# Kernel optimization log

Hardware: AMD Instinct MI355X
Metric: run time of the kernel (lower is better)

Reference implementation:

```python
import jax, jax.numpy as jnp
import numpy as np


def bilinear_sampler(img, coords):
    """RAFT-style bilinear sampler: grid_sample(align_corners=True, zero padding)
    at absolute pixel coords. img: (N,C,H,W); coords: (N,Ho,Wo,2) with (x,y).
    Returns (N,C,Ho,Wo)."""
    N, C, H, W = img.shape
    x = coords[..., 0]
    y = coords[..., 1]
    x0f = jnp.floor(x)
    y0f = jnp.floor(y)
    wx = x - x0f  # fractional weights
    wy = y - y0f
    x0 = x0f.astype(jnp.int32)
    y0 = y0f.astype(jnp.int32)
    x1 = x0 + 1
    y1 = y0 + 1
    n = jnp.arange(N)[:, None, None]  # (N,1,1) batch index

    def gather(yi, xi):
        valid = (xi >= 0) & (xi < W) & (yi >= 0) & (yi < H)
        v = img[n, :, jnp.clip(yi, 0, H - 1), jnp.clip(xi, 0, W - 1)]  # (N,Ho,Wo,C)
        return v * valid[..., None].astype(img.dtype)

    out = (gather(y0, x0) * ((1 - wy) * (1 - wx))[..., None]
           + gather(y0, x1) * ((1 - wy) * wx)[..., None]
           + gather(y1, x0) * (wy * (1 - wx))[..., None]
           + gather(y1, x1) * (wy * wx)[..., None])
    return out.transpose(0, 3, 1, 2)


def setup_inputs() -> dict:
    key = jax.random.key(0)
    k1, k2, k3 = jax.random.split(key, 3)
    B, H, W, heads = 4, 64, 64, 1
    cost_maps = jax.random.normal(k1, (B * H * W, heads, H, W), dtype=jnp.float32)
    # pixel coords uniform in [0, W-1]
    coords0 = jax.random.uniform(k2, (B, 2, H, W), dtype=jnp.float32) * (W - 1)
    coords1 = jax.random.uniform(k3, (B, 2, H, W), dtype=jnp.float32) * (W - 1)
    return {"cost_maps": cost_maps, "coords0": coords0, "coords1": coords1}


def reference(cost_maps, coords0, coords1):
    BH1W1, heads, H2, W2 = cost_maps.shape
    B, _, H1, W1 = coords1.shape
    # first gather: sample each (h1,w1,head) cost map at coords1
    cm = cost_maps.reshape(B, H1 * W1 * heads, H2, W2)
    corr = bilinear_sampler(cm, coords1.transpose(0, 2, 3, 1))  # (B, H1*W1*heads, H1, W1)
    # rearrange 'b (h1 w1 heads) h2 w2 -> (b h2 w2) heads h1 w1'
    corr = corr.reshape(B, H1, W1, heads, H2, W2)
    corr = corr.transpose(0, 4, 5, 3, 1, 2).reshape(B * H2 * W2, heads, H1, W1)
    # second gather: 9x9 window around coords0 (faithful to torch meshgrid(dy,dx))
    r = 4
    dx = jnp.linspace(-r, r, 2 * r + 1, dtype=jnp.float32)
    dy = jnp.linspace(-r, r, 2 * r + 1, dtype=jnp.float32)
    delta = jnp.stack(jnp.meshgrid(dy, dx, indexing="ij"), axis=-1)  # (9,9,2)
    centroid = coords0.transpose(0, 2, 3, 1).reshape(BH1W1, 1, 1, 2)
    coords = centroid + delta[None]  # (BH1W1, 9, 9, 2)
    corr = bilinear_sampler(corr, coords)  # (BH1W1, heads, 9, 9)
    out = corr.reshape(B, H1, W1, -1).transpose(0, 3, 1, 2)  # (B, heads*81, H1, W1)
    return out
```

## Files before the change

kernel.cpp:

```cpp
#include <hip/hip_runtime.h>


#define PIX     16
#define THREADS 256

__global__ __launch_bounds__(THREADS, 4)
void rce_kernel(const float* __restrict__ cost,
                const float* __restrict__ coords0,
                const float* __restrict__ coords1,
                float* __restrict__ out) {
    const int tid = threadIdx.x;
    const int P   = blockIdx.x * PIX;
    const int b   = P >> 12;
    const int i   = (P >> 6) & 63;
    const int j0  = P & 63;

    __shared__ int   s_pos[PIX][4];
    __shared__ float s_w[PIX][4];
    __shared__ int   s_x0i[PIX], s_y0i[PIX];
    __shared__ int   s_rx[PIX][9], s_ry[PIX][9];
    __shared__ float s_fx[PIX][9], s_fy[PIX][9];
    __shared__ float s_F[PIX][101];

    if (tid < PIX) {
        const int j = j0 + tid;
        const int cbase = (b * 2) * 4096 + i * 64 + j;

        float x1 = coords1[cbase];
        float y1 = coords1[cbase + 4096];
        float x1f = floorf(x1), y1f = floorf(y1);
        int   xi = (int)x1f,    yi = (int)y1f;
        float wx = x1 - x1f,    wy = y1 - y1f;
        int x0c = min(max(xi, 0), 63),     x1c = min(max(xi + 1, 0), 63);
        int y0c = min(max(yi, 0), 63),     y1c = min(max(yi + 1, 0), 63);
        float vx0 = ((unsigned)xi       < 64u) ? 1.f : 0.f;
        float vx1 = ((unsigned)(xi + 1) < 64u) ? 1.f : 0.f;
        float vy0 = ((unsigned)yi       < 64u) ? 1.f : 0.f;
        float vy1 = ((unsigned)(yi + 1) < 64u) ? 1.f : 0.f;
        s_pos[tid][0] = y0c * 64 + x0c;  s_w[tid][0] = (1.f - wy) * (1.f - wx) * vy0 * vx0;
        s_pos[tid][1] = y0c * 64 + x1c;  s_w[tid][1] = (1.f - wy) * wx         * vy0 * vx1;
        s_pos[tid][2] = y1c * 64 + x0c;  s_w[tid][2] = wy         * (1.f - wx) * vy1 * vx0;
        s_pos[tid][3] = y1c * 64 + x1c;  s_w[tid][3] = wy         * wx         * vy1 * vx1;

        float x0 = coords0[cbase];
        float y0 = coords0[cbase + 4096];
        int x0i = (int)floorf(x0);
        int y0i = (int)floorf(y0);
        s_x0i[tid] = x0i;
        s_y0i[tid] = y0i;
#pragma unroll
        for (int a = 0; a < 9; ++a) {
            float X  = x0 + (float)(a - 4);
            float Xf = floorf(X);
            s_rx[tid][a] = (int)Xf - (x0i - 4);
            s_fx[tid][a] = X - Xf;
            float Y  = y0 + (float)(a - 4);
            float Yf = floorf(Y);
            s_ry[tid][a] = (int)Yf - (y0i - 4);
            s_fy[tid][a] = Y - Yf;
        }
    }
    __syncthreads();

    const float* cmb = cost + (size_t)b * 4096 * 4096;
#pragma unroll
    for (int it = 0; it < (PIX * 100 + THREADS - 1) / THREADS; ++it) {
        int task = it * THREADS + tid;
        if (task < PIX * 100) {
            int px = task & (PIX - 1);
            int e  = task >> 4;
            int yy = e / 10;
            int xx = e - yy * 10;
            int X = s_x0i[px] - 4 + xx;
            int Y = s_y0i[px] - 4 + yy;
            float F = 0.f;
            if (((unsigned)X < 64u) & ((unsigned)Y < 64u)) {
                const float* map = cmb + ((size_t)(Y * 64 + X) << 12);
                F = s_w[px][0] * map[s_pos[px][0]]
                  + s_w[px][1] * map[s_pos[px][1]]
                  + s_w[px][2] * map[s_pos[px][2]]
                  + s_w[px][3] * map[s_pos[px][3]];
            }
            s_F[px][e] = F;
        }
    }
    __syncthreads();

    const int px  = tid & (PIX - 1);
    const int chb = tid >> 4;
    const size_t obase = (((size_t)b * 81) * 64 + i) * 64 + (size_t)(j0 + px);
#pragma unroll
    for (int it = 0; it < (81 + (THREADS / PIX) - 1) / (THREADS / PIX); ++it) {
        int ch = it * (THREADS / PIX) + chb;
        if (ch < 81) {
            int a  = ch / 9;
            int bb = ch - a * 9;
            int   rx = s_rx[px][a];  float fx = s_fx[px][a];
            int   ry = s_ry[px][bb]; float fy = s_fy[px][bb];
            float f00 = (((unsigned)ry       < 10u) & ((unsigned)rx       < 10u)) ? s_F[px][ry * 10 + rx]           : 0.f;
            float f01 = (((unsigned)ry       < 10u) & ((unsigned)(rx + 1) < 10u)) ? s_F[px][ry * 10 + rx + 1]       : 0.f;
            float f10 = (((unsigned)(ry + 1) < 10u) & ((unsigned)rx       < 10u)) ? s_F[px][(ry + 1) * 10 + rx]     : 0.f;
            float f11 = (((unsigned)(ry + 1) < 10u) & ((unsigned)(rx + 1) < 10u)) ? s_F[px][(ry + 1) * 10 + rx + 1] : 0.f;
            float v = (1.f - fy) * ((1.f - fx) * f00 + fx * f01)
                    + fy         * ((1.f - fx) * f10 + fx * f11);
            out[obase + (size_t)ch * 4096] = v;
        }
    }
}

extern "C" void kernel_launch(void* const* d_in, const int* in_sizes, int n_in,
                              void* d_out, int out_size, void* d_ws, size_t ws_size,
                              hipStream_t stream) {
    const float* cost    = (const float*)d_in[0];
    const float* coords0 = (const float*)d_in[1];
    const float* coords1 = (const float*)d_in[2];
    float* out = (float*)d_out;

    const int total_px = 4 * 64 * 64;
    dim3 grid(total_px / PIX), block(THREADS);
    rce_kernel<<<grid, block, 0, stream>>>(cost, coords0, coords1, out);
}
```

Measured before the change: 65.74 us.

## Invert gather into per-cost-map streaming with bucketed pixel lists

Replaces the per-pixel scattered gather of 100 cost maps with a four-kernel pipeline. The new pipeline zeroes the workspace, buckets pixels by their coords0 cell using atomics, streams each 64x64 cost map into shared memory once, and evaluates every pixel whose 10x10 window touches that map. A final kernel performs the 9x9 bilinear window from the staged F buffer. It aims to replace uncoalesced random global reads with coalesced full-map loads, at the cost of reading the entire cost tensor, extra launches and workspace traffic, and a fixed per-cell list capacity.

```diff
diff --git a/kernel.cpp b/kernel.cpp
--- a/kernel.cpp
+++ b/kernel.cpp
@@ -1,97 +1,147 @@
 #include <hip/hip_runtime.h>
 
 
-#define PIX     16
-#define THREADS 256
+#define CAP 64
+#define FSTR 104
 
-__global__ __launch_bounds__(THREADS, 4)
-void rce_kernel(const float* __restrict__ cost,
-                const float* __restrict__ coords0,
-                const float* __restrict__ coords1,
-                float* __restrict__ out) {
+#define OFF_CNT   0u
+#define OFF_LIST  65536u
+#define OFF_POS   4259840u
+#define OFF_WGT   4521984u
+#define OFF_F     4784128u
+
+__global__ __launch_bounds__(256)
+void k0_zero(int* __restrict__ cnt, float* __restrict__ F) {
+    int t = blockIdx.x * 256 + threadIdx.x;
+    if (t < 16384) cnt[t] = 0;
+    for (int i = t; i < 16384 * 100; i += gridDim.x * 256) F[i] = 0.f;
+}
+
+__global__ __launch_bounds__(256)
+void k1_setup(const float* __restrict__ coords0, const float* __restrict__ coords1,
+              int* __restrict__ cnt, int* __restrict__ list,
+              int4* __restrict__ pos, float4* __restrict__ wgt) {
+    int pid = blockIdx.x * 256 + threadIdx.x;
+    int b   = pid >> 12;
+    int cb  = b * 8192 + (pid & 4095);
+
+    float x1 = coords1[cb];
+    float y1 = coords1[cb + 4096];
+    float x1f = floorf(x1), y1f = floorf(y1);
+    int   xi = (int)x1f,    yi = (int)y1f;
+    float wx = x1 - x1f,    wy = y1 - y1f;
+    int x0c = min(max(xi, 0), 63),     x1c = min(max(xi + 1, 0), 63);
+    int y0c = min(max(yi, 0), 63),     y1c = min(max(yi + 1, 0), 63);
+    float vx0 = ((unsigned)xi       < 64u) ? 1.f : 0.f;
+    float vx1 = ((unsigned)(xi + 1) < 64u) ? 1.f : 0.f;
+    float vy0 = ((unsigned)yi       < 64u) ? 1.f : 0.f;
+    float vy1 = ((unsigned)(yi + 1) < 64u) ? 1.f : 0.f;
+    pos[pid] = make_int4(y0c * 64 + x0c, y0c * 64 + x1c, y1c * 64 + x0c, y1c * 64 + x1c);
+    wgt[pid] = make_float4((1.f - wy) * (1.f - wx) * vy0 * vx0,
+                           (1.f - wy) * wx         * vy0 * vx1,
+                           wy         * (1.f - wx) * vy1 * vx0,
+                           wy         * wx         * vy1 * vx1);
+
+    float x0 = coords0[cb];
+    float y0 = coords0[cb + 4096];
+    int x0i = (int)floorf(x0);
+    int y0i = (int)floorf(y0);
+    int cell = (b << 12) | (y0i << 6) | x0i;
+    int slot = atomicAdd(&cnt[cell], 1);
+    if (slot < CAP) list[cell * CAP + slot] = pid;
+}
+
+__global__ __launch_bounds__(256, 8)
+void k2_corr(const float* __restrict__ cost,
+             const int* __restrict__ cnt, const int* __restrict__ list,
+             const int4* __restrict__ pos, const float4* __restrict__ wgt,
+             float* __restrict__ F) {
+    const int bid = blockIdx.x;
+    const int b = bid >> 12, Y = (bid >> 6) & 63, X = bid & 63;
     const int tid = threadIdx.x;
-    const int P   = blockIdx.x * PIX;
-    const int b   = P >> 12;
-    const int i   = (P >> 6) & 63;
-    const int j0  = P & 63;
 
-    __shared__ int   s_pos[PIX][4];
-    __shared__ float s_w[PIX][4];
-    __shared__ int   s_x0i[PIX], s_y0i[PIX];
-    __shared__ int   s_rx[PIX][9], s_ry[PIX][9];
-    __shared__ float s_fx[PIX][9], s_fy[PIX][9];
-    __shared__ float s_F[PIX][101];
+    __shared__ float s_map[4096];
 
-    if (tid < PIX) {
-        const int j = j0 + tid;
-        const int cbase = (b * 2) * 4096 + i * 64 + j;
+    const float4* m4 = (const float4*)(cost + (size_t)bid * 4096);
+    float4 v[4];
+#pragma unroll
+    for (int k = 0; k < 4; ++k) v[k] = m4[tid + k * 256];
 
-        float x1 = coords1[cbase];
-        float y1 = coords1[cbase + 4096];
-        float x1f = floorf(x1), y1f = floorf(y1);
-        int   xi = (int)x1f,    yi = (int)y1f;
-        float wx = x1 - x1f,    wy = y1 - y1f;
-        int x0c = min(max(xi, 0), 63),     x1c = min(max(xi + 1, 0), 63);
-        int y0c = min(max(yi, 0), 63),     y1c = min(max(yi + 1, 0), 63);
-        float vx0 = ((unsigned)xi       < 64u) ? 1.f : 0.f;
-        float vx1 = ((unsigned)(xi + 1) < 64u) ? 1.f : 0.f;
-        float vy0 = ((unsigned)yi       < 64u) ? 1.f : 0.f;
-        float vy1 = ((unsigned)(yi + 1) < 64u) ? 1.f : 0.f;
-        s_pos[tid][0] = y0c * 64 + x0c;  s_w[tid][0] = (1.f - wy) * (1.f - wx) * vy0 * vx0;
-        s_pos[tid][1] = y0c * 64 + x1c;  s_w[tid][1] = (1.f - wy) * wx         * vy0 * vx1;
-        s_pos[tid][2] = y1c * 64 + x0c;  s_w[tid][2] = wy         * (1.f - wx) * vy1 * vx0;
-        s_pos[tid][3] = y1c * 64 + x1c;  s_w[tid][3] = wy         * wx         * vy1 * vx1;
+    int n = 0, cell = 0, e = 0;
+    if (tid < 100) {
+        int dy = tid / 10, dx = tid - dy * 10;
+        int cy = Y - 5 + dy, cx = X - 5 + dx;
+        e = (9 - dy) * 10 + (9 - dx);
+        if (((unsigned)cy < 64u) & ((unsigned)cx < 64u)) {
+            cell = (b << 12) | (cy << 6) | cx;
+            n = min(cnt[cell], CAP);
+        }
+    }
 
-        float x0 = coords0[cbase];
-        float y0 = coords0[cbase + 4096];
+#pragma unroll
+    for (int k = 0; k < 4; ++k) ((float4*)s_map)[tid + k * 256] = v[k];
+    __syncthreads();
+
+    for (int k = 0; k < n; ++k) {
+        int   pid = list[cell * CAP + k];
+        int4  P   = pos[pid];
+        float4 Wt = wgt[pid];
+        float f = Wt.x * s_map[P.x] + Wt.y * s_map[P.y]
+                + Wt.z * s_map[P.z] + Wt.w * s_map[P.w];
+        F[pid * 100 + e] = f;
+    }
+}
+
+__global__ __launch_bounds__(256)
+void k3_out(const float* __restrict__ coords0, const float* __restrict__ F,
+            float* __restrict__ out) {
+    const int tid = threadIdx.x;
+    const int P0  = blockIdx.x * 8;
+    const int b = P0 >> 12, i = (P0 >> 6) & 63, j0 = P0 & 63;
+
+    __shared__ int   s_rx[8][9], s_ry[8][9];
+    __shared__ float s_fx[8][9], s_fy[8][9];
+    __shared__ float s_F[8][FSTR];
+
+    if (tid < 8) {
+        int cb = b * 8192 + ((P0 + tid) & 4095);
+        float x0 = coords0[cb];
+        float y0 = coords0[cb + 4096];
         int x0i = (int)floorf(x0);
         int y0i = (int)floorf(y0);
-        s_x0i[tid] = x0i;
-        s_y0i[tid] = y0i;
 #pragma unroll
         for (int a = 0; a < 9; ++a) {
-            float X  = x0 + (float)(a - 4);
-            float Xf = floorf(X);
+            float Xv = x0 + (float)(a - 4);
+            float Xf = floorf(Xv);
             s_rx[tid][a] = (int)Xf - (x0i - 4);
-            s_fx[tid][a] = X - Xf;
-            float Y  = y0 + (float)(a - 4);
-            float Yf = floorf(Y);
+            s_fx[tid][a] = Xv - Xf;
+            float Yv = y0 + (float)(a - 4);
+            float Yf = floorf(Yv);
             s_ry[tid][a] = (int)Yf - (y0i - 4);
-            s_fy[tid][a] = Y - Yf;
+            s_fy[tid][a] = Yv - Yf;
         }
+    }
+
+    {
+        int px = tid >> 5, l = tid & 31;
+        const float* Fr = F + (size_t)(P0 + px) * 100;
+        float t0 = Fr[l];
+        float t1 = Fr[l + 32];
+        float t2 = Fr[l + 64];
+        float t3 = (l < 4) ? Fr[l + 96] : 0.f;
+        s_F[px][l]      = t0;
+        s_F[px][l + 32] = t1;
+        s_F[px][l + 64] = t2;
+        if (l < 4) s_F[px][l + 96] = t3;
     }
     __syncthreads();
 
-    const float* cmb = cost + (size_t)b * 4096 * 4096;
-#pragma unroll
-    for (int it = 0; it < (PIX * 100 + THREADS - 1) / THREADS; ++it) {
-        int task = it * THREADS + tid;
-        if (task < PIX * 100) {
-            int px = task & (PIX - 1);
-            int e  = task >> 4;
-            int yy = e / 10;
-            int xx = e - yy * 10;
-            int X = s_x0i[px] - 4 + xx;
-            int Y = s_y0i[px] - 4 + yy;
-            float F = 0.f;
-            if (((unsigned)X < 64u) & ((unsigned)Y < 64u)) {
-                const float* map = cmb + ((size_t)(Y * 64 + X) << 12);
-                F = s_w[px][0] * map[s_pos[px][0]]
-                  + s_w[px][1] * map[s_pos[px][1]]
-                  + s_w[px][2] * map[s_pos[px][2]]
-                  + s_w[px][3] * map[s_pos[px][3]];
-            }
-            s_F[px][e] = F;
-        }
-    }
-    __syncthreads();
-
-    const int px  = tid & (PIX - 1);
-    const int chb = tid >> 4;
+    const int px  = tid & 7;
+    const int chb = tid >> 3;
     const size_t obase = (((size_t)b * 81) * 64 + i) * 64 + (size_t)(j0 + px);
 #pragma unroll
-    for (int it = 0; it < (81 + (THREADS / PIX) - 1) / (THREADS / PIX); ++it) {
-        int ch = it * (THREADS / PIX) + chb;
+    for (int r = 0; r < 3; ++r) {
+        int ch = r * 32 + chb;
         if (ch < 81) {
             int a  = ch / 9;
             int bb = ch - a * 9;
@@ -116,7 +166,15 @@
     const float* coords1 = (const float*)d_in[2];
     float* out = (float*)d_out;
 
-    const int total_px = 4 * 64 * 64;
-    dim3 grid(total_px / PIX), block(THREADS);
-    rce_kernel<<<grid, block, 0, stream>>>(cost, coords0, coords1, out);
+    char* ws = (char*)d_ws;
+    int*    cnt  = (int*)   (ws + OFF_CNT);
+    int*    list = (int*)   (ws + OFF_LIST);
+    int4*   pos  = (int4*)  (ws + OFF_POS);
+    float4* wgt  = (float4*)(ws + OFF_WGT);
+    float*  F    = (float*) (ws + OFF_F);
+
+    k0_zero <<<2048, 256, 0, stream>>>(cnt, F);
+    k1_setup<<<64,   256, 0, stream>>>(coords0, coords1, cnt, list, pos, wgt);
+    k2_corr <<<16384,256, 0, stream>>>(cost, cnt, list, pos, wgt, F);
+    k3_out  <<<2048, 256, 0, stream>>>(coords0, F, out);
 }
```

Measured after the change: 84.26 us. 1.28x slower.
